# Kernel optimization log

Hardware: AMD Instinct MI355X
Metric: run time of the kernel (lower is better)

Reference implementation:

```python
import jax, jax.numpy as jnp
import numpy as np

N = 8192
IN_DIM = 128
OUT_DIM = 64
ALPHA = 0.2  # leaky_relu negative slope
NEG_BIG = -9e15


def setup_inputs() -> dict:
    key = jax.random.key(0)
    k1, k2, k3, k4, k5 = jax.random.split(key, 5)
    h = jax.random.normal(k1, (N, IN_DIM), dtype=jnp.float32)
    adj = jax.random.randint(k2, (N, N), 0, 2, dtype=jnp.int32)
    w = jax.random.normal(k3, (IN_DIM, OUT_DIM), dtype=jnp.float32) * (1.414 / np.sqrt(IN_DIM))
    a = jax.random.normal(k4, (2 * OUT_DIM, 1), dtype=jnp.float32) * 0.1
    b = jax.random.uniform(k5, (OUT_DIM,), dtype=jnp.float32, minval=-1.0, maxval=1.0) / np.sqrt(OUT_DIM)
    return {"h": h, "adj": adj, "w": w, "a": a, "b": b}


def reference(h, adj, w, a, b):
    # wh: [N, D_out]
    wh = h @ w
    d = wh.shape[1]
    # broadcast attention logits: e[i,j] = leaky_relu(wh[i]@a1 + wh[j]@a2)
    wh1 = wh @ a[:d]   # [N, 1]
    wh2 = wh @ a[d:]   # [N, 1]
    e = jax.nn.leaky_relu(wh1 + wh2.T, negative_slope=ALPHA)  # [N, N]
    # adjacency mask + row softmax (dropout=0 / eval mode -> identity)
    att = jnp.where(adj > 0, e, NEG_BIG)
    att = jax.nn.softmax(att, axis=1)
    h_prime = att @ wh + b  # [N, D_out]
    return jax.nn.elu(h_prime)  # concat=True -> elu
```

## Files before the change

kernel.cpp:

```cpp
#include <hip/hip_runtime.h>
#include <hip/hip_bf16.h>

#define NN 8192
#define D_IN 128
#define D_OUT 64
#define GAT_ALPHA 0.2f
#define LOG2E 1.4426950408889634f
#define JT 256
#define NTILES (NN / JT)

typedef __attribute__((ext_vector_type(4))) float f32x4;
typedef __attribute__((ext_vector_type(8))) short short8;

static __device__ __forceinline__ unsigned short f32_bf16(float f) {
    unsigned u = __builtin_bit_cast(unsigned, f);
    u += 0x7fffu + ((u >> 16) & 1u);
    return (unsigned short)(u >> 16);
}

__global__ __launch_bounds__(256) void gat_prep(
    const float* __restrict__ h, const float* __restrict__ w,
    const float* __restrict__ a,
    unsigned short* __restrict__ whB, float* __restrict__ wh1p,
    float* __restrict__ wh2p)
{
    __shared__ float hs[16 * 128];
    __shared__ float whs[16][64];
    const int t = threadIdx.x;
    const int i0 = blockIdx.x * 16;

    const float* hsrc = h + (size_t)i0 * D_IN;
    *(float4*)(hs + t * 8)     = *(const float4*)(hsrc + t * 8);
    *(float4*)(hs + t * 8 + 4) = *(const float4*)(hsrc + t * 8 + 4);
    __syncthreads();

    const int r  = t >> 4;
    const int og = (t & 15) * 4;
    f32x4 acc = {0.f, 0.f, 0.f, 0.f};
    for (int k = 0; k < D_IN; ++k) {
        float hv = hs[r * 128 + k];
        float4 wv = *(const float4*)(w + k * D_OUT + og);
        acc[0] += hv * wv.x; acc[1] += hv * wv.y;
        acc[2] += hv * wv.z; acc[3] += hv * wv.w;
    }
    whs[r][og]     = acc[0];
    whs[r][og + 1] = acc[1];
    whs[r][og + 2] = acc[2];
    whs[r][og + 3] = acc[3];

    float p1 = acc[0]*a[og] + acc[1]*a[og+1] + acc[2]*a[og+2] + acc[3]*a[og+3];
    float p2 = acc[0]*a[64+og] + acc[1]*a[64+og+1] + acc[2]*a[64+og+2] + acc[3]*a[64+og+3];
    #pragma unroll
    for (int m = 1; m < 16; m <<= 1) {
        p1 += __shfl_xor(p1, m);
        p2 += __shfl_xor(p2, m);
    }
    if ((t & 15) == 0) {
        wh1p[i0 + r] = p1 * LOG2E;
        wh2p[i0 + r] = p2 * LOG2E;
    }
    __syncthreads();

    {
        const int half = t >> 7;
        const int dim  = (t >> 1) & 63;
        const int e0   = (t & 1) * 4;
        ushort4 v;
        v.x = f32_bf16(whs[half * 8 + e0 + 0][dim]);
        v.y = f32_bf16(whs[half * 8 + e0 + 1][dim]);
        v.z = f32_bf16(whs[half * 8 + e0 + 2][dim]);
        v.w = f32_bf16(whs[half * 8 + e0 + 3][dim]);
        *(ushort4*)(whB + (size_t)(i0 / 8 + half) * 512 + dim * 8 + e0) = v;
    }
}

__global__ __launch_bounds__(512) void gat_main(
    const int* __restrict__ adj, const unsigned short* __restrict__ whB,
    const float* __restrict__ wh1p, const float* __restrict__ wh2p,
    const float* __restrict__ bias, float* __restrict__ out)
{
    __shared__ alignas(16) int adjs[2][16][260];
    __shared__ float nums8[8][16][64];
    __shared__ float dens8[8][16];

    const int t    = threadIdx.x;
    const int wv   = t >> 6;
    const int lane = t & 63;
    const int il   = lane & 15;
    const int kg   = lane >> 4;
    const int i0   = blockIdx.x * 16;

    const float c = wh1p[i0 + il];

    f32x4 acc0 = {0,0,0,0}, acc1 = {0,0,0,0}, acc2 = {0,0,0,0}, acc3 = {0,0,0,0};
    float den = 0.f;

    const int r0 = wv * 2;

    {
        const int* g0 = adj + (size_t)(i0 + r0) * NN + lane * 4;
        const int* g1 = adj + (size_t)(i0 + r0 + 1) * NN + lane * 4;
        __builtin_amdgcn_global_load_lds(
            (const __attribute__((address_space(1))) void*)g0,
            (__attribute__((address_space(3))) void*)&adjs[0][r0][0], 16, 0, 0);
        __builtin_amdgcn_global_load_lds(
            (const __attribute__((address_space(1))) void*)g1,
            (__attribute__((address_space(3))) void*)&adjs[0][r0 + 1][0], 16, 0, 0);
    }

    for (int tg = 0; tg < NTILES; ++tg) {
        const int b = tg & 1;
        __syncthreads();

        if (tg + 1 < NTILES) {
            const int jn = (tg + 1) * JT;
            const int* g0 = adj + (size_t)(i0 + r0) * NN + jn + lane * 4;
            const int* g1 = adj + (size_t)(i0 + r0 + 1) * NN + jn + lane * 4;
            __builtin_amdgcn_global_load_lds(
                (const __attribute__((address_space(1))) void*)g0,
                (__attribute__((address_space(3))) void*)&adjs[b ^ 1][r0][0], 16, 0, 0);
            __builtin_amdgcn_global_load_lds(
                (const __attribute__((address_space(1))) void*)g1,
                (__attribute__((address_space(3))) void*)&adjs[b ^ 1][r0 + 1][0], 16, 0, 0);
        }

        const int jl = wv * 32 + kg * 8;
        const int jg = tg * JT + jl;
        int4 ad0 = *(const int4*)&adjs[b][il][jl];
        int4 ad1 = *(const int4*)&adjs[b][il][jl + 4];
        float4 w20 = *(const float4*)(wh2p + jg);
        float4 w21 = *(const float4*)(wh2p + jg + 4);

        const unsigned short* bb =
            whB + (size_t)(tg * 32 + wv * 4 + kg) * 512 + il * 8;
        short8 b0 = *(const short8*)(bb);
        short8 b1 = *(const short8*)(bb + 128);
        short8 b2 = *(const short8*)(bb + 256);
        short8 b3 = *(const short8*)(bb + 384);

        short8 af;
        {
            float x, p;
            x = c + w20.x; x = fmaxf(x, GAT_ALPHA * x); p = __builtin_amdgcn_exp2f(x);
            p = ad0.x ? p : 0.f; den += p; af[0] = (short)f32_bf16(p);
            x = c + w20.y; x = fmaxf(x, GAT_ALPHA * x); p = __builtin_amdgcn_exp2f(x);
            p = ad0.y ? p : 0.f; den += p; af[1] = (short)f32_bf16(p);
            x = c + w20.z; x = fmaxf(x, GAT_ALPHA * x); p = __builtin_amdgcn_exp2f(x);
            p = ad0.z ? p : 0.f; den += p; af[2] = (short)f32_bf16(p);
            x = c + w20.w; x = fmaxf(x, GAT_ALPHA * x); p = __builtin_amdgcn_exp2f(x);
            p = ad0.w ? p : 0.f; den += p; af[3] = (short)f32_bf16(p);
            x = c + w21.x; x = fmaxf(x, GAT_ALPHA * x); p = __builtin_amdgcn_exp2f(x);
            p = ad1.x ? p : 0.f; den += p; af[4] = (short)f32_bf16(p);
            x = c + w21.y; x = fmaxf(x, GAT_ALPHA * x); p = __builtin_amdgcn_exp2f(x);
            p = ad1.y ? p : 0.f; den += p; af[5] = (short)f32_bf16(p);
            x = c + w21.z; x = fmaxf(x, GAT_ALPHA * x); p = __builtin_amdgcn_exp2f(x);
            p = ad1.z ? p : 0.f; den += p; af[6] = (short)f32_bf16(p);
            x = c + w21.w; x = fmaxf(x, GAT_ALPHA * x); p = __builtin_amdgcn_exp2f(x);
            p = ad1.w ? p : 0.f; den += p; af[7] = (short)f32_bf16(p);
        }

        acc0 = __builtin_amdgcn_mfma_f32_16x16x32_bf16(af, b0, acc0, 0, 0, 0);
        acc1 = __builtin_amdgcn_mfma_f32_16x16x32_bf16(af, b1, acc1, 0, 0, 0);
        acc2 = __builtin_amdgcn_mfma_f32_16x16x32_bf16(af, b2, acc2, 0, 0, 0);
        acc3 = __builtin_amdgcn_mfma_f32_16x16x32_bf16(af, b3, acc3, 0, 0, 0);
    }

    den += __shfl_xor(den, 16);
    den += __shfl_xor(den, 32);
    if (kg == 0) dens8[wv][il] = den;

    #pragma unroll
    for (int q = 0; q < 4; ++q) {
        nums8[wv][kg * 4 + q][0 * 16 + il] = acc0[q];
        nums8[wv][kg * 4 + q][1 * 16 + il] = acc1[q];
        nums8[wv][kg * 4 + q][2 * 16 + il] = acc2[q];
        nums8[wv][kg * 4 + q][3 * 16 + il] = acc3[q];
    }
    __syncthreads();

    for (int idx = t; idx < 16 * 64; idx += 512) {
        const int rr = idx >> 6, cc = idx & 63;
        float s = 0.f, d = 0.f;
        #pragma unroll
        for (int wq = 0; wq < 8; ++wq) { s += nums8[wq][rr][cc]; d += dens8[wq][rr]; }
        float val = s / d + bias[cc];
        out[(size_t)(i0 + rr) * D_OUT + cc] =
            val > 0.f ? val : (__builtin_amdgcn_exp2f(val * LOG2E) - 1.f);
    }
}

extern "C" void kernel_launch(void* const* d_in, const int* in_sizes, int n_in,
                              void* d_out, int out_size, void* d_ws, size_t ws_size,
                              hipStream_t stream) {
    const float* h   = (const float*)d_in[0];
    const int*   adj = (const int*)d_in[1];
    const float* w   = (const float*)d_in[2];
    const float* a   = (const float*)d_in[3];
    const float* b   = (const float*)d_in[4];
    float* out = (float*)d_out;

    char* ws = (char*)d_ws;
    unsigned short* whB = (unsigned short*)ws;
    float* wh1p = (float*)(ws + (size_t)D_OUT * NN * 2);
    float* wh2p = (float*)(ws + (size_t)D_OUT * NN * 2 + NN * 4);

    gat_prep<<<NN / 16, 256, 0, stream>>>(h, w, a, whB, wh1p, wh2p);
    gat_main<<<NN / 16, 512, 0, stream>>>(adj, whB, wh1p, wh2p, b, out);
}
```

Before: 77.92 us.

## Split columns per wave with private 4-deep adjacency pipeline, removing block barriers

Each of 4 waves now owns a contiguous 2048-column slice and streams its own adjacency tiles through a private 4-stage LDS ring. Manual vmcnt waits replace the per-tile __syncthreads, and a swizzled LDS layout avoids bank conflicts. Block size drops from 512 to 256 threads. The aim is to remove block-wide barrier stalls and keep more adjacency loads in flight. In exchange there are fewer threads per block and the code depends on hand-tuned waitcnt counts and sched barriers being correct.

```diff
diff --git a/kernel.cpp b/kernel.cpp
--- a/kernel.cpp
+++ b/kernel.cpp
@@ -6,8 +6,6 @@
 #define D_OUT 64
 #define GAT_ALPHA 0.2f
 #define LOG2E 1.4426950408889634f
-#define JT 256
-#define NTILES (NN / JT)
 
 typedef __attribute__((ext_vector_type(4))) float f32x4;
 typedef __attribute__((ext_vector_type(8))) short short8;
@@ -74,14 +72,59 @@
     }
 }
 
-__global__ __launch_bounds__(512) void gat_main(
+#define AF_LANE(PV, AD, IDX)                                                    \
+    do { float x_ = c + (PV);                                                   \
+         x_ = fmaxf(x_, GAT_ALPHA * x_);                                        \
+         float p_ = __builtin_amdgcn_exp2f(x_);                                 \
+         p_ = (AD) ? p_ : 0.f; den += p_;                                       \
+         af[IDX] = (short)f32_bf16(p_); } while (0)
+
+#define TILE(n, WN, DO_STAGE) do {                                              \
+    const int j0_ = jbase + (n) * 32;                                           \
+    float4 w20 = *(const float4*)(wh2p + j0_ + kg * 8);                         \
+    float4 w21 = *(const float4*)(wh2p + j0_ + kg * 8 + 4);                     \
+    const unsigned short* bb_ = whB + (size_t)(j0_ / 8 + kg) * 512 + il * 8;    \
+    short8 b0 = *(const short8*)(bb_);                                          \
+    short8 b1 = *(const short8*)(bb_ + 128);                                    \
+    short8 b2 = *(const short8*)(bb_ + 256);                                    \
+    short8 b3 = *(const short8*)(bb_ + 384);                                    \
+    __builtin_amdgcn_sched_barrier(0);                                          \
+    if (DO_STAGE) {                                                             \
+        const int tl_ = (n) + 3;                                                \
+        const int off_ = tl_ * 32;                                              \
+        __builtin_amdgcn_global_load_lds(                                       \
+            (const __attribute__((address_space(1))) void*)(g0 + off_),         \
+            (__attribute__((address_space(3))) void*)&adjs[wv][tl_ & 3][0],     \
+            16, 0, 0);                                                          \
+        __builtin_amdgcn_global_load_lds(                                       \
+            (const __attribute__((address_space(1))) void*)(g1 + off_),         \
+            (__attribute__((address_space(3))) void*)&adjs[wv][tl_ & 3][64],    \
+            16, 0, 0);                                                          \
+    }                                                                           \
+    asm volatile("s_waitcnt vmcnt(" #WN ")" ::: "memory");                      \
+    __builtin_amdgcn_sched_barrier(0);                                          \
+    const int4* base_ = &adjs[wv][(n) & 3][0];                                  \
+    int4 ad0 = base_[uA];                                                       \
+    int4 ad1 = base_[uB];                                                       \
+    short8 af;                                                                  \
+    AF_LANE(w20.x, ad0.x, 0); AF_LANE(w20.y, ad0.y, 1);                         \
+    AF_LANE(w20.z, ad0.z, 2); AF_LANE(w20.w, ad0.w, 3);                         \
+    AF_LANE(w21.x, ad1.x, 4); AF_LANE(w21.y, ad1.y, 5);                         \
+    AF_LANE(w21.z, ad1.z, 6); AF_LANE(w21.w, ad1.w, 7);                         \
+    acc0 = __builtin_amdgcn_mfma_f32_16x16x32_bf16(af, b0, acc0, 0, 0, 0);      \
+    acc1 = __builtin_amdgcn_mfma_f32_16x16x32_bf16(af, b1, acc1, 0, 0, 0);      \
+    acc2 = __builtin_amdgcn_mfma_f32_16x16x32_bf16(af, b2, acc2, 0, 0, 0);      \
+    acc3 = __builtin_amdgcn_mfma_f32_16x16x32_bf16(af, b3, acc3, 0, 0, 0);      \
+} while (0)
+
+__global__ __launch_bounds__(256) void gat_main(
     const int* __restrict__ adj, const unsigned short* __restrict__ whB,
     const float* __restrict__ wh1p, const float* __restrict__ wh2p,
     const float* __restrict__ bias, float* __restrict__ out)
 {
-    __shared__ alignas(16) int adjs[2][16][260];
-    __shared__ float nums8[8][16][64];
-    __shared__ float dens8[8][16];
+    __shared__ int4  adjs[4][4][128];
+    __shared__ float nums4[4][16][64];
+    __shared__ float dens4[4][16];
 
     const int t    = threadIdx.x;
     const int wv   = t >> 6;
@@ -89,100 +132,59 @@
     const int il   = lane & 15;
     const int kg   = lane >> 4;
     const int i0   = blockIdx.x * 16;
+    const int jbase = wv * 2048;
 
     const float c = wh1p[i0 + il];
+
+    const int srow = lane >> 3;
+    const int scol = ((lane & 7) + 8 - srow) & 7;
+    const int* g0 = adj + (size_t)(i0 + srow) * NN + jbase + scol * 4;
+    const int* g1 = adj + (size_t)(i0 + 8 + srow) * NN + jbase + scol * 4;
+
+    const int uA = il * 8 + ((2 * kg + il) & 7);
+    const int uB = il * 8 + ((2 * kg + 1 + il) & 7);
 
     f32x4 acc0 = {0,0,0,0}, acc1 = {0,0,0,0}, acc2 = {0,0,0,0}, acc3 = {0,0,0,0};
     float den = 0.f;
 
-    const int r0 = wv * 2;
-
-    {
-        const int* g0 = adj + (size_t)(i0 + r0) * NN + lane * 4;
-        const int* g1 = adj + (size_t)(i0 + r0 + 1) * NN + lane * 4;
+    #pragma unroll
+    for (int tl = 0; tl < 3; ++tl) {
+        const int off = tl * 32;
         __builtin_amdgcn_global_load_lds(
-            (const __attribute__((address_space(1))) void*)g0,
-            (__attribute__((address_space(3))) void*)&adjs[0][r0][0], 16, 0, 0);
+            (const __attribute__((address_space(1))) void*)(g0 + off),
+            (__attribute__((address_space(3))) void*)&adjs[wv][tl][0], 16, 0, 0);
         __builtin_amdgcn_global_load_lds(
-            (const __attribute__((address_space(1))) void*)g1,
-            (__attribute__((address_space(3))) void*)&adjs[0][r0 + 1][0], 16, 0, 0);
-    }
-
-    for (int tg = 0; tg < NTILES; ++tg) {
-        const int b = tg & 1;
-        __syncthreads();
-
-        if (tg + 1 < NTILES) {
-            const int jn = (tg + 1) * JT;
-            const int* g0 = adj + (size_t)(i0 + r0) * NN + jn + lane * 4;
-            const int* g1 = adj + (size_t)(i0 + r0 + 1) * NN + jn + lane * 4;
-            __builtin_amdgcn_global_load_lds(
-                (const __attribute__((address_space(1))) void*)g0,
-                (__attribute__((address_space(3))) void*)&adjs[b ^ 1][r0][0], 16, 0, 0);
-            __builtin_amdgcn_global_load_lds(
-                (const __attribute__((address_space(1))) void*)g1,
-                (__attribute__((address_space(3))) void*)&adjs[b ^ 1][r0 + 1][0], 16, 0, 0);
-        }
-
-        const int jl = wv * 32 + kg * 8;
-        const int jg = tg * JT + jl;
-        int4 ad0 = *(const int4*)&adjs[b][il][jl];
-        int4 ad1 = *(const int4*)&adjs[b][il][jl + 4];
-        float4 w20 = *(const float4*)(wh2p + jg);
-        float4 w21 = *(const float4*)(wh2p + jg + 4);
-
-        const unsigned short* bb =
-            whB + (size_t)(tg * 32 + wv * 4 + kg) * 512 + il * 8;
-        short8 b0 = *(const short8*)(bb);
-        short8 b1 = *(const short8*)(bb + 128);
-        short8 b2 = *(const short8*)(bb + 256);
-        short8 b3 = *(const short8*)(bb + 384);
-
-        short8 af;
-        {
-            float x, p;
-            x = c + w20.x; x = fmaxf(x, GAT_ALPHA * x); p = __builtin_amdgcn_exp2f(x);
-            p = ad0.x ? p : 0.f; den += p; af[0] = (short)f32_bf16(p);
-            x = c + w20.y; x = fmaxf(x, GAT_ALPHA * x); p = __builtin_amdgcn_exp2f(x);
-            p = ad0.y ? p : 0.f; den += p; af[1] = (short)f32_bf16(p);
-            x = c + w20.z; x = fmaxf(x, GAT_ALPHA * x); p = __builtin_amdgcn_exp2f(x);
-            p = ad0.z ? p : 0.f; den += p; af[2] = (short)f32_bf16(p);
-            x = c + w20.w; x = fmaxf(x, GAT_ALPHA * x); p = __builtin_amdgcn_exp2f(x);
-            p = ad0.w ? p : 0.f; den += p; af[3] = (short)f32_bf16(p);
-            x = c + w21.x; x = fmaxf(x, GAT_ALPHA * x); p = __builtin_amdgcn_exp2f(x);
-            p = ad1.x ? p : 0.f; den += p; af[4] = (short)f32_bf16(p);
-            x = c + w21.y; x = fmaxf(x, GAT_ALPHA * x); p = __builtin_amdgcn_exp2f(x);
-            p = ad1.y ? p : 0.f; den += p; af[5] = (short)f32_bf16(p);
-            x = c + w21.z; x = fmaxf(x, GAT_ALPHA * x); p = __builtin_amdgcn_exp2f(x);
-            p = ad1.z ? p : 0.f; den += p; af[6] = (short)f32_bf16(p);
-            x = c + w21.w; x = fmaxf(x, GAT_ALPHA * x); p = __builtin_amdgcn_exp2f(x);
-            p = ad1.w ? p : 0.f; den += p; af[7] = (short)f32_bf16(p);
-        }
-
-        acc0 = __builtin_amdgcn_mfma_f32_16x16x32_bf16(af, b0, acc0, 0, 0, 0);
-        acc1 = __builtin_amdgcn_mfma_f32_16x16x32_bf16(af, b1, acc1, 0, 0, 0);
-        acc2 = __builtin_amdgcn_mfma_f32_16x16x32_bf16(af, b2, acc2, 0, 0, 0);
-        acc3 = __builtin_amdgcn_mfma_f32_16x16x32_bf16(af, b3, acc3, 0, 0, 0);
-    }
+            (const __attribute__((address_space(1))) void*)(g1 + off),
+            (__attribute__((address_space(3))) void*)&adjs[wv][tl][64], 16, 0, 0);
+    }
+
+    TILE(0, 12, true);
+    TILE(1, 18, true);
+    for (int n = 2; n <= 60; ++n) {
+        TILE(n, 24, true);
+    }
+    TILE(61, 22, false);
+    TILE(62, 20, false);
+    TILE(63, 18, false);
 
     den += __shfl_xor(den, 16);
     den += __shfl_xor(den, 32);
-    if (kg == 0) dens8[wv][il] = den;
+    if (kg == 0) dens4[wv][il] = den;
 
     #pragma unroll
     for (int q = 0; q < 4; ++q) {
-        nums8[wv][kg * 4 + q][0 * 16 + il] = acc0[q];
-        nums8[wv][kg * 4 + q][1 * 16 + il] = acc1[q];
-        nums8[wv][kg * 4 + q][2 * 16 + il] = acc2[q];
-        nums8[wv][kg * 4 + q][3 * 16 + il] = acc3[q];
+        nums4[wv][kg * 4 + q][0 * 16 + il] = acc0[q];
+        nums4[wv][kg * 4 + q][1 * 16 + il] = acc1[q];
+        nums4[wv][kg * 4 + q][2 * 16 + il] = acc2[q];
+        nums4[wv][kg * 4 + q][3 * 16 + il] = acc3[q];
     }
     __syncthreads();
 
-    for (int idx = t; idx < 16 * 64; idx += 512) {
+    for (int idx = t; idx < 16 * 64; idx += 256) {
         const int rr = idx >> 6, cc = idx & 63;
         float s = 0.f, d = 0.f;
         #pragma unroll
-        for (int wq = 0; wq < 8; ++wq) { s += nums8[wq][rr][cc]; d += dens8[wq][rr]; }
+        for (int wq = 0; wq < 4; ++wq) { s += nums4[wq][rr][cc]; d += dens4[wq][rr]; }
         float val = s / d + bias[cc];
         out[(size_t)(i0 + rr) * D_OUT + cc] =
             val > 0.f ? val : (__builtin_amdgcn_exp2f(val * LOG2E) - 1.f);
@@ -205,5 +207,5 @@
     float* wh2p = (float*)(ws + (size_t)D_OUT * NN * 2 + NN * 4);
 
     gat_prep<<<NN / 16, 256, 0, stream>>>(h, w, a, whB, wh1p, wh2p);
-    gat_main<<<NN / 16, 512, 0, stream>>>(adj, whB, wh1p, wh2p, b, out);
-}
+    gat_main<<<NN / 16, 256, 0, stream>>>(adj, whB, wh1p, wh2p, b, out);
+}
```

Result: no change. 77.65 us (-0.4%).

## Compress adjacency to bitmask in prep kernel and process 32 rows per block

Applied to the files above, without the earlier changes.

Adds an adjacency-to-bitmask pass fused into the prep kernel, so the main kernel reads a 1-bit-per-edge mask instead of 32-bit ints. The main kernel now handles 32 rows per block across 256 blocks and loads the whole bitmask tile and all of wh2 into LDS up front. Each whB fragment now feeds two MFMAs, which halves B-operand traffic per row. The risks are that the prep pass still reads the full int adjacency, that grid occupancy drops to 256 blocks, and that the large LDS footprint limits residency.

```diff
diff --git a/kernel.cpp b/kernel.cpp
--- a/kernel.cpp
+++ b/kernel.cpp
@@ -6,8 +6,6 @@
 #define D_OUT 64
 #define GAT_ALPHA 0.2f
 #define LOG2E 1.4426950408889634f
-#define JT 256
-#define NTILES (NN / JT)
 
 typedef __attribute__((ext_vector_type(4))) float f32x4;
 typedef __attribute__((ext_vector_type(8))) short short8;
@@ -18,7 +16,8 @@
     return (unsigned short)(u >> 16);
 }
 
-__global__ __launch_bounds__(256) void gat_prep(
+__global__ __launch_bounds__(256) void gat_pre(
+    const int* __restrict__ adj, unsigned char* __restrict__ bm,
     const float* __restrict__ h, const float* __restrict__ w,
     const float* __restrict__ a,
     unsigned short* __restrict__ whB, float* __restrict__ wh1p,
@@ -27,7 +26,29 @@
     __shared__ float hs[16 * 128];
     __shared__ float whs[16][64];
     const int t = threadIdx.x;
-    const int i0 = blockIdx.x * 16;
+
+    if (blockIdx.x < 2048) {
+        const size_t base = (size_t)blockIdx.x * 256 + t;
+        #pragma unroll
+        for (int it = 0; it < 16; ++it) {
+            const size_t G = (size_t)it * 524288 + base;
+            const int4* p = (const int4*)(adj + G * 8);
+            int4 v0 = p[0], v1 = p[1];
+            unsigned b = 0;
+            b |= (unsigned)(v0.x > 0) << 0;
+            b |= (unsigned)(v0.y > 0) << 1;
+            b |= (unsigned)(v0.z > 0) << 2;
+            b |= (unsigned)(v0.w > 0) << 3;
+            b |= (unsigned)(v1.x > 0) << 4;
+            b |= (unsigned)(v1.y > 0) << 5;
+            b |= (unsigned)(v1.z > 0) << 6;
+            b |= (unsigned)(v1.w > 0) << 7;
+            bm[G] = (unsigned char)b;
+        }
+        return;
+    }
+
+    const int i0 = (blockIdx.x - 2048) * 16;
 
     const float* hsrc = h + (size_t)i0 * D_IN;
     *(float4*)(hs + t * 8)     = *(const float4*)(hsrc + t * 8);
@@ -74,117 +95,124 @@
     }
 }
 
+static __device__ __forceinline__ short8 pack8_bf16(const float* p) {
+    union { unsigned int u[4]; short8 s; } r;
+    asm("v_cvt_pk_bf16_f32 %0, %1, %2" : "=v"(r.u[0]) : "v"(p[0]), "v"(p[1]));
+    asm("v_cvt_pk_bf16_f32 %0, %1, %2" : "=v"(r.u[1]) : "v"(p[2]), "v"(p[3]));
+    asm("v_cvt_pk_bf16_f32 %0, %1, %2" : "=v"(r.u[2]) : "v"(p[4]), "v"(p[5]));
+    asm("v_cvt_pk_bf16_f32 %0, %1, %2" : "=v"(r.u[3]) : "v"(p[6]), "v"(p[7]));
+    return r.s;
+}
+
 __global__ __launch_bounds__(512) void gat_main(
-    const int* __restrict__ adj, const unsigned short* __restrict__ whB,
+    const unsigned int* __restrict__ bm, const unsigned short* __restrict__ whB,
     const float* __restrict__ wh1p, const float* __restrict__ wh2p,
     const float* __restrict__ bias, float* __restrict__ out)
 {
-    __shared__ alignas(16) int adjs[2][16][260];
-    __shared__ float nums8[8][16][64];
-    __shared__ float dens8[8][16];
+    __shared__ alignas(16) char smem[66560];
+    unsigned int (*bmlds)[260] = (unsigned int(*)[260])smem;
+    float* w2lds = (float*)(smem + 33280);
+    float (*nums)[32][64] = (float(*)[32][64])smem;
+    float (*dens)[32] = (float(*)[32])(smem + 65536);
 
     const int t    = threadIdx.x;
     const int wv   = t >> 6;
     const int lane = t & 63;
     const int il   = lane & 15;
     const int kg   = lane >> 4;
-    const int i0   = blockIdx.x * 16;
-
-    const float c = wh1p[i0 + il];
-
-    f32x4 acc0 = {0,0,0,0}, acc1 = {0,0,0,0}, acc2 = {0,0,0,0}, acc3 = {0,0,0,0};
-    float den = 0.f;
-
-    const int r0 = wv * 2;
+    const int r0   = blockIdx.x * 32;
 
     {
-        const int* g0 = adj + (size_t)(i0 + r0) * NN + lane * 4;
-        const int* g1 = adj + (size_t)(i0 + r0 + 1) * NN + lane * 4;
-        __builtin_amdgcn_global_load_lds(
-            (const __attribute__((address_space(1))) void*)g0,
-            (__attribute__((address_space(3))) void*)&adjs[0][r0][0], 16, 0, 0);
-        __builtin_amdgcn_global_load_lds(
-            (const __attribute__((address_space(1))) void*)g1,
-            (__attribute__((address_space(3))) void*)&adjs[0][r0 + 1][0], 16, 0, 0);
-    }
-
-    for (int tg = 0; tg < NTILES; ++tg) {
-        const int b = tg & 1;
-        __syncthreads();
-
-        if (tg + 1 < NTILES) {
-            const int jn = (tg + 1) * JT;
-            const int* g0 = adj + (size_t)(i0 + r0) * NN + jn + lane * 4;
-            const int* g1 = adj + (size_t)(i0 + r0 + 1) * NN + jn + lane * 4;
-            __builtin_amdgcn_global_load_lds(
-                (const __attribute__((address_space(1))) void*)g0,
-                (__attribute__((address_space(3))) void*)&adjs[b ^ 1][r0][0], 16, 0, 0);
-            __builtin_amdgcn_global_load_lds(
-                (const __attribute__((address_space(1))) void*)g1,
-                (__attribute__((address_space(3))) void*)&adjs[b ^ 1][r0 + 1][0], 16, 0, 0);
-        }
-
-        const int jl = wv * 32 + kg * 8;
-        const int jg = tg * JT + jl;
-        int4 ad0 = *(const int4*)&adjs[b][il][jl];
-        int4 ad1 = *(const int4*)&adjs[b][il][jl + 4];
-        float4 w20 = *(const float4*)(wh2p + jg);
-        float4 w21 = *(const float4*)(wh2p + jg + 4);
-
-        const unsigned short* bb =
-            whB + (size_t)(tg * 32 + wv * 4 + kg) * 512 + il * 8;
+        const uint4*  bmg = (const uint4*)(bm + r0 * 256);
+        const float4* w2g = (const float4*)wh2p;
+        #pragma unroll
+        for (int q = 0; q < 4; ++q) {
+            const int C = q * 512 + t;
+            uint4 v = bmg[C];
+            const int rr = C >> 6, cc = (C & 63) * 4;
+            *(uint4*)&bmlds[rr][cc] = v;
+            float4 wv2 = w2g[C];
+            *(float4*)&w2lds[C * 4] = wv2;
+        }
+    }
+    __syncthreads();
+
+    const float c0 = wh1p[r0 + il];
+    const float c1 = wh1p[r0 + 16 + il];
+    const int shk = kg * 8;
+
+    f32x4 acc[2][4] = {};
+    float den0 = 0.f, den1 = 0.f;
+
+    #pragma unroll 4
+    for (int n = 0; n < 32; ++n) {
+        const int jd = wv * 32 + n;
+        const int j0 = jd * 32;
+
+        unsigned int m0 = bmlds[il][jd] >> shk;
+        unsigned int m1 = bmlds[16 + il][jd] >> shk;
+        float4 W0 = *(const float4*)&w2lds[j0 + kg * 8];
+        float4 W1 = *(const float4*)&w2lds[j0 + kg * 8 + 4];
+
+        const unsigned short* bb = whB + (size_t)(j0 / 8 + kg) * 512 + il * 8;
         short8 b0 = *(const short8*)(bb);
         short8 b1 = *(const short8*)(bb + 128);
         short8 b2 = *(const short8*)(bb + 256);
         short8 b3 = *(const short8*)(bb + 384);
 
-        short8 af;
-        {
-            float x, p;
-            x = c + w20.x; x = fmaxf(x, GAT_ALPHA * x); p = __builtin_amdgcn_exp2f(x);
-            p = ad0.x ? p : 0.f; den += p; af[0] = (short)f32_bf16(p);
-            x = c + w20.y; x = fmaxf(x, GAT_ALPHA * x); p = __builtin_amdgcn_exp2f(x);
-            p = ad0.y ? p : 0.f; den += p; af[1] = (short)f32_bf16(p);
-            x = c + w20.z; x = fmaxf(x, GAT_ALPHA * x); p = __builtin_amdgcn_exp2f(x);
-            p = ad0.z ? p : 0.f; den += p; af[2] = (short)f32_bf16(p);
-            x = c + w20.w; x = fmaxf(x, GAT_ALPHA * x); p = __builtin_amdgcn_exp2f(x);
-            p = ad0.w ? p : 0.f; den += p; af[3] = (short)f32_bf16(p);
-            x = c + w21.x; x = fmaxf(x, GAT_ALPHA * x); p = __builtin_amdgcn_exp2f(x);
-            p = ad1.x ? p : 0.f; den += p; af[4] = (short)f32_bf16(p);
-            x = c + w21.y; x = fmaxf(x, GAT_ALPHA * x); p = __builtin_amdgcn_exp2f(x);
-            p = ad1.y ? p : 0.f; den += p; af[5] = (short)f32_bf16(p);
-            x = c + w21.z; x = fmaxf(x, GAT_ALPHA * x); p = __builtin_amdgcn_exp2f(x);
-            p = ad1.z ? p : 0.f; den += p; af[6] = (short)f32_bf16(p);
-            x = c + w21.w; x = fmaxf(x, GAT_ALPHA * x); p = __builtin_amdgcn_exp2f(x);
-            p = ad1.w ? p : 0.f; den += p; af[7] = (short)f32_bf16(p);
-        }
-
-        acc0 = __builtin_amdgcn_mfma_f32_16x16x32_bf16(af, b0, acc0, 0, 0, 0);
-        acc1 = __builtin_amdgcn_mfma_f32_16x16x32_bf16(af, b1, acc1, 0, 0, 0);
-        acc2 = __builtin_amdgcn_mfma_f32_16x16x32_bf16(af, b2, acc2, 0, 0, 0);
-        acc3 = __builtin_amdgcn_mfma_f32_16x16x32_bf16(af, b3, acc3, 0, 0, 0);
-    }
-
-    den += __shfl_xor(den, 16);
-    den += __shfl_xor(den, 32);
-    if (kg == 0) dens8[wv][il] = den;
-
+        float wvv[8] = {W0.x, W0.y, W0.z, W0.w, W1.x, W1.y, W1.z, W1.w};
+        float p0[8], p1[8];
+        #pragma unroll
+        for (int e = 0; e < 8; ++e) {
+            float x = c0 + wvv[e];
+            x = fmaxf(x, GAT_ALPHA * x);
+            float p = __builtin_amdgcn_exp2f(x);
+            p = (m0 & (1u << e)) ? p : 0.f;
+            den0 += p; p0[e] = p;
+            float y = c1 + wvv[e];
+            y = fmaxf(y, GAT_ALPHA * y);
+            float q = __builtin_amdgcn_exp2f(y);
+            q = (m1 & (1u << e)) ? q : 0.f;
+            den1 += q; p1[e] = q;
+        }
+        short8 af0 = pack8_bf16(p0);
+        short8 af1 = pack8_bf16(p1);
+
+        acc[0][0] = __builtin_amdgcn_mfma_f32_16x16x32_bf16(af0, b0, acc[0][0], 0, 0, 0);
+        acc[1][0] = __builtin_amdgcn_mfma_f32_16x16x32_bf16(af1, b0, acc[1][0], 0, 0, 0);
+        acc[0][1] = __builtin_amdgcn_mfma_f32_16x16x32_bf16(af0, b1, acc[0][1], 0, 0, 0);
+        acc[1][1] = __builtin_amdgcn_mfma_f32_16x16x32_bf16(af1, b1, acc[1][1], 0, 0, 0);
+        acc[0][2] = __builtin_amdgcn_mfma_f32_16x16x32_bf16(af0, b2, acc[0][2], 0, 0, 0);
+        acc[1][2] = __builtin_amdgcn_mfma_f32_16x16x32_bf16(af1, b2, acc[1][2], 0, 0, 0);
+        acc[0][3] = __builtin_amdgcn_mfma_f32_16x16x32_bf16(af0, b3, acc[0][3], 0, 0, 0);
+        acc[1][3] = __builtin_amdgcn_mfma_f32_16x16x32_bf16(af1, b3, acc[1][3], 0, 0, 0);
+    }
+
+    den0 += __shfl_xor(den0, 16); den0 += __shfl_xor(den0, 32);
+    den1 += __shfl_xor(den1, 16); den1 += __shfl_xor(den1, 32);
+
+    __syncthreads();
+
+    if (kg == 0) { dens[wv][il] = den0; dens[wv][16 + il] = den1; }
     #pragma unroll
     for (int q = 0; q < 4; ++q) {
-        nums8[wv][kg * 4 + q][0 * 16 + il] = acc0[q];
-        nums8[wv][kg * 4 + q][1 * 16 + il] = acc1[q];
-        nums8[wv][kg * 4 + q][2 * 16 + il] = acc2[q];
-        nums8[wv][kg * 4 + q][3 * 16 + il] = acc3[q];
-    }
-    __syncthreads();
-
-    for (int idx = t; idx < 16 * 64; idx += 512) {
+        #pragma unroll
+        for (int d = 0; d < 4; ++d) {
+            nums[wv][kg * 4 + q][d * 16 + il]      = acc[0][d][q];
+            nums[wv][16 + kg * 4 + q][d * 16 + il] = acc[1][d][q];
+        }
+    }
+    __syncthreads();
+
+    #pragma unroll
+    for (int k = 0; k < 4; ++k) {
+        const int idx = k * 512 + t;
         const int rr = idx >> 6, cc = idx & 63;
-        float s = 0.f, d = 0.f;
-        #pragma unroll
-        for (int wq = 0; wq < 8; ++wq) { s += nums8[wq][rr][cc]; d += dens8[wq][rr]; }
-        float val = s / d + bias[cc];
-        out[(size_t)(i0 + rr) * D_OUT + cc] =
+        float s = 0.f, dd = 0.f;
+        #pragma unroll
+        for (int w8 = 0; w8 < 8; ++w8) { s += nums[w8][rr][cc]; dd += dens[w8][rr]; }
+        float val = s / dd + bias[cc];
+        out[(size_t)(r0 + rr) * D_OUT + cc] =
             val > 0.f ? val : (__builtin_amdgcn_exp2f(val * LOG2E) - 1.f);
     }
 }
@@ -203,7 +231,8 @@
     unsigned short* whB = (unsigned short*)ws;
     float* wh1p = (float*)(ws + (size_t)D_OUT * NN * 2);
     float* wh2p = (float*)(ws + (size_t)D_OUT * NN * 2 + NN * 4);
-
-    gat_prep<<<NN / 16, 256, 0, stream>>>(h, w, a, whB, wh1p, wh2p);
-    gat_main<<<NN / 16, 512, 0, stream>>>(adj, whB, wh1p, wh2p, b, out);
-}
+    unsigned char* bm = (unsigned char*)(ws + (size_t)D_OUT * NN * 2 + NN * 8);
+
+    gat_pre<<<2560, 256, 0, stream>>>(adj, bm, h, w, a, whB, wh1p, wh2p);
+    gat_main<<<256, 512, 0, stream>>>((const unsigned int*)bm, whB, wh1p, wh2p, b, out);
+}
```

Result: no change. 79.41 us (+1.9%).
